# Kernel tuning notes

Measured on AMD Instinct MI355X. Metric: run time of the kernel, lower is better.

The kernel has to match this reference:

```python
import jax, jax.numpy as jnp
import numpy as np

B, N, D, OUT, ED = 8, 256, 128, 128, 1

def setup_inputs() -> dict:
    key = jax.random.key(0)
    ks = jax.random.split(key, 10)
    in2 = 2 * D + ED  # 257
    s = lambda f: 1.0 / np.sqrt(f)
    return {
        "h": jax.random.normal(ks[0], (B, N, D), dtype=jnp.float32),
        "adj": jax.random.randint(ks[1], (B, N, N), 0, 2, dtype=jnp.int32),
        "dist_matrix": jax.random.uniform(ks[2], (B, N, N), dtype=jnp.float32),
        "Wm1": jax.random.uniform(ks[3], (in2, OUT), minval=-s(in2), maxval=s(in2)),
        "bm1": jnp.zeros((OUT,), jnp.float32),
        "Wm2": jax.random.uniform(ks[4], (OUT, OUT), minval=-s(OUT), maxval=s(OUT)),
        "bm2": jnp.zeros((OUT,), jnp.float32),
        "Wa": jax.random.uniform(ks[5], (in2, 1), minval=-s(in2), maxval=s(in2)),
        "ba": jnp.zeros((1,), jnp.float32),
        "Wu": jax.random.uniform(ks[6], (D + OUT, OUT), minval=-s(D + OUT), maxval=s(D + OUT)),
        "bu": jnp.zeros((OUT,), jnp.float32),
    }

def reference(h, adj, dist_matrix, Wm1, bm1, Wm2, bm2, Wa, ba, Wu, bu):
    # h: (B,N,D); adj,dist: (B,N,N)
    Bb, Nn, Dd = h.shape
    h_i = jnp.broadcast_to(h[:, :, None, :], (Bb, Nn, Nn, Dd))
    h_j = jnp.broadcast_to(h[:, None, :, :], (Bb, Nn, Nn, Dd))
    d_ij = dist_matrix[..., None]
    msg_input = jnp.concatenate([h_i, h_j, d_ij], axis=-1)  # (B,N,N,2D+1)
    # message MLP: Linear -> ReLU -> Linear
    msg = jax.nn.relu(msg_input @ Wm1 + bm1) @ Wm2 + bm2    # (B,N,N,OUT)
    # attention MLP: Linear -> LeakyReLU(0.2)
    attn = jax.nn.leaky_relu(msg_input @ Wa + ba, 0.2)      # (B,N,N,1)
    mask = adj[..., None].astype(msg.dtype)                  # (B,N,N,1)
    attn = jnp.where(mask == 0, jnp.asarray(-1e9, attn.dtype), attn)
    attn = jax.nn.softmax(attn, axis=2)                      # softmax over j
    agg = jnp.sum(attn * msg * mask, axis=2)                 # (B,N,OUT)
    h_new = jax.nn.relu(jnp.concatenate([h, agg], axis=-1) @ Wu + bu)
    return h_new
```

## Files before the change

### kernel.cpp

```cpp
#include <hip/hip_runtime.h>

#define NN 256
#define DD 128
#define OC 128

__device__ __forceinline__ float bcastf(float x, int lane) {
    return __int_as_float(__builtin_amdgcn_readlane(__float_as_int(x), lane));
}

__global__ __launch_bounds__(256) void k1_pre(
    const float* __restrict__ h, const float* __restrict__ Wm1,
    const float* __restrict__ Wa, const float* __restrict__ bm1,
    const float* __restrict__ Wu, const float* __restrict__ ba,
    float* __restrict__ pre, float* __restrict__ aiv, float* __restrict__ ajv)
{
    const int tid  = threadIdx.x;
    const int l    = tid & 63;
    const int w    = tid >> 6;
    const int row0 = blockIdx.x * 4;

    const float2* h2 = (const float2*)h;
    float2 hr[4];
    #pragma unroll
    for (int r = 0; r < 4; ++r) hr[r] = h2[(row0 + r) * 64 + l];

    if (w == 3) {
        const float2* Wa2 = (const float2*)Wa;
        const float2 wt = Wa2[l], wb = Wa2[64 + l];
        float vi[4], vj[4];
        #pragma unroll
        for (int r = 0; r < 4; ++r) {
            vi[r] = hr[r].x * wt.x + hr[r].y * wt.y;
            vj[r] = hr[r].x * wb.x + hr[r].y * wb.y;
        }
        #pragma unroll
        for (int o = 1; o < 64; o <<= 1) {
            #pragma unroll
            for (int r = 0; r < 4; ++r) {
                vi[r] += __shfl_xor(vi[r], o, 64);
                vj[r] += __shfl_xor(vj[r], o, 64);
            }
        }
        if (l == 0) {
            const float b0 = ba[0];
            #pragma unroll
            for (int r = 0; r < 4; ++r) {
                aiv[row0 + r] = vi[r] + b0;
                ajv[row0 + r] = vj[r];
            }
        }
        return;
    }

    const float2* W2 = (w == 0) ? (const float2*)Wm1
                     : (w == 1) ? (const float2*)Wm1 + DD * 64
                                : (const float2*)Wu;

    float2 acc[4];
    #pragma unroll
    for (int r = 0; r < 4; ++r) acc[r] = make_float2(0.f, 0.f);

    #pragma unroll 4
    for (int m = 0; m < 64; ++m) {
        const float2 w0 = W2[(2 * m) * 64 + l];
        const float2 w1 = W2[(2 * m + 1) * 64 + l];
        #pragma unroll
        for (int r = 0; r < 4; ++r) {
            const float hx = bcastf(hr[r].x, m);
            const float hy = bcastf(hr[r].y, m);
            acc[r].x = fmaf(hx, w0.x, fmaf(hy, w1.x, acc[r].x));
            acc[r].y = fmaf(hx, w0.y, fmaf(hy, w1.y, acc[r].y));
        }
    }
    if (w == 0) {
        const float2 bb = ((const float2*)bm1)[l];
        #pragma unroll
        for (int r = 0; r < 4; ++r) { acc[r].x += bb.x; acc[r].y += bb.y; }
    }
    float2* pre2 = (float2*)pre;
    #pragma unroll
    for (int r = 0; r < 4; ++r)
        pre2[(row0 + r) * 192 + w * 64 + l] = acc[r];
}

__global__ __launch_bounds__(256) void k2_main(
    const int* __restrict__ adj, const float* __restrict__ dist,
    const float* __restrict__ Wm1, const float* __restrict__ Wa,
    const float* __restrict__ pre,
    const float* __restrict__ aiv, const float* __restrict__ ajv,
    const float* __restrict__ Wm2, const float* __restrict__ bm2,
    const float* __restrict__ Wu,  const float* __restrict__ bu,
    float* __restrict__ out)
{
    const int tid  = threadIdx.x;
    const int l    = tid & 63;
    const int w    = tid >> 6;
    const int row0 = blockIdx.x * 4;
    const int row  = row0 + w;
    const int b    = row >> 8;

    __shared__ float t_sh[4][128];
    __shared__ float agg_sh[4][128];
    __shared__ float sf_sh[4];

    const int4   mk4 = ((const int4*)  (adj  + row * NN))[l];
    const float4 dv4 = ((const float4*)(dist + row * NN))[l];
    const float4 aj4 = ((const float4*)(ajv  + b   * NN))[l];
    const float  ai  = aiv[row];
    const float  dc  = Wa[2 * DD];

    float lg[4];
    lg[0] = ai + aj4.x + dv4.x * dc;
    lg[1] = ai + aj4.y + dv4.y * dc;
    lg[2] = ai + aj4.z + dv4.z * dc;
    lg[3] = ai + aj4.w + dv4.w * dc;
    #pragma unroll
    for (int c = 0; c < 4; ++c) lg[c] = (lg[c] >= 0.f) ? lg[c] : 0.2f * lg[c];
    const int mk[4] = {mk4.x, mk4.y, mk4.z, mk4.w};

    float m = -1e9f;
    #pragma unroll
    for (int c = 0; c < 4; ++c) if (mk[c]) m = fmaxf(m, lg[c]);
    #pragma unroll
    for (int o = 1; o < 64; o <<= 1) m = fmaxf(m, __shfl_xor(m, o, 64));

    float e[4], s = 0.f;
    #pragma unroll
    for (int c = 0; c < 4; ++c) { e[c] = mk[c] ? __expf(lg[c] - m) : 0.f; s += e[c]; }
    #pragma unroll
    for (int o = 1; o < 64; o <<= 1) s += __shfl_xor(s, o, 64);
    const float inv = (s > 0.f) ? (1.0f / s) : 0.f;
    float wj0 = e[0] * inv, wj1 = e[1] * inv, wj2 = e[2] * inv, wj3 = e[3] * inv;

    const float2* pre2 = (const float2*)pre;
    const float2  pa   = pre2[row * 192 + l];
    const float2  wd1  = ((const float2*)Wm1)[2 * DD * 64 + l];
    const float2* pBb  = pre2 + (size_t)b * NN * 192 + 64;

    float2 acc = make_float2(0.f, 0.f);
    for (int p = 0; p < 64; ++p) {
        const float sw0 = bcastf(wj0, p), sd0 = bcastf(dv4.x, p);
        const float sw1 = bcastf(wj1, p), sd1 = bcastf(dv4.y, p);
        const float sw2 = bcastf(wj2, p), sd2 = bcastf(dv4.z, p);
        const float sw3 = bcastf(wj3, p), sd3 = bcastf(dv4.w, p);
        const int jb = 4 * p;
        if (sw0 != 0.f) {
            const float2 pb = pBb[jb * 192 + l];
            const float vx = fmaf(sd0, wd1.x, pa.x + pb.x);
            const float vy = fmaf(sd0, wd1.y, pa.y + pb.y);
            acc.x = fmaf(sw0, fmaxf(vx, 0.f), acc.x);
            acc.y = fmaf(sw0, fmaxf(vy, 0.f), acc.y);
        }
        if (sw1 != 0.f) {
            const float2 pb = pBb[(jb + 1) * 192 + l];
            const float vx = fmaf(sd1, wd1.x, pa.x + pb.x);
            const float vy = fmaf(sd1, wd1.y, pa.y + pb.y);
            acc.x = fmaf(sw1, fmaxf(vx, 0.f), acc.x);
            acc.y = fmaf(sw1, fmaxf(vy, 0.f), acc.y);
        }
        if (sw2 != 0.f) {
            const float2 pb = pBb[(jb + 2) * 192 + l];
            const float vx = fmaf(sd2, wd1.x, pa.x + pb.x);
            const float vy = fmaf(sd2, wd1.y, pa.y + pb.y);
            acc.x = fmaf(sw2, fmaxf(vx, 0.f), acc.x);
            acc.y = fmaf(sw2, fmaxf(vy, 0.f), acc.y);
        }
        if (sw3 != 0.f) {
            const float2 pb = pBb[(jb + 3) * 192 + l];
            const float vx = fmaf(sd3, wd1.x, pa.x + pb.x);
            const float vy = fmaf(sd3, wd1.y, pa.y + pb.y);
            acc.x = fmaf(sw3, fmaxf(vx, 0.f), acc.x);
            acc.y = fmaf(sw3, fmaxf(vy, 0.f), acc.y);
        }
    }
    t_sh[w][2 * l]     = acc.x;
    t_sh[w][2 * l + 1] = acc.y;
    if (l == 0) sf_sh[w] = (s > 0.f) ? 1.f : 0.f;
    __syncthreads();

    const int c   = 32 * w + (l & 31);
    const int rsl = l >> 5;
    float a[2];
    #pragma unroll
    for (int pass = 0; pass < 2; ++pass) {
        const int r = 2 * pass + rsl;
        float av = 0.f;
        #pragma unroll 8
        for (int k = 0; k < 128; ++k)
            av = fmaf(t_sh[r][k], Wm2[k * OC + c], av);
        a[pass] = fmaf(bm2[c], sf_sh[r], av);
    }
    #pragma unroll
    for (int pass = 0; pass < 2; ++pass)
        agg_sh[2 * pass + rsl][c] = a[pass];
    __syncthreads();

    const float buc = bu[c];
    #pragma unroll
    for (int pass = 0; pass < 2; ++pass) {
        const int r = 2 * pass + rsl;
        float ov = 0.f;
        #pragma unroll 8
        for (int k = 0; k < 128; ++k)
            ov = fmaf(agg_sh[r][k], Wu[(DD + k) * OC + c], ov);
        const float hu = pre[(row0 + r) * 384 + 256 + c];
        out[(row0 + r) * OC + c] = fmaxf(ov + hu + buc, 0.f);
    }
}

extern "C" void kernel_launch(void* const* d_in, const int* in_sizes, int n_in,
                              void* d_out, int out_size, void* d_ws, size_t ws_size,
                              hipStream_t stream) {
    const float* h    = (const float*)d_in[0];
    const int*   adj  = (const int*)  d_in[1];
    const float* dist = (const float*)d_in[2];
    const float* Wm1  = (const float*)d_in[3];
    const float* bm1  = (const float*)d_in[4];
    const float* Wm2  = (const float*)d_in[5];
    const float* bm2  = (const float*)d_in[6];
    const float* Wa   = (const float*)d_in[7];
    const float* ba   = (const float*)d_in[8];
    const float* Wu   = (const float*)d_in[9];
    const float* bu   = (const float*)d_in[10];
    float* out = (float*)d_out;

    float* pre = (float*)d_ws;
    float* aiv = pre + 2048 * 384;
    float* ajv = aiv + 2048;

    k1_pre <<<512, 256, 0, stream>>>(h, Wm1, Wa, bm1, Wu, ba, pre, aiv, ajv);
    k2_main<<<512, 256, 0, stream>>>(adj, dist, Wm1, Wa, pre, aiv, ajv,
                                     Wm2, bm2, Wu, bu, out);
}
```

Before: 132.2 us.

## Split each row's neighbor loop across two waves and double the grid

```diff
diff --git a/kernel.cpp b/kernel.cpp
--- a/kernel.cpp
+++ b/kernel.cpp
@@ -17,26 +17,26 @@
     const int tid  = threadIdx.x;
     const int l    = tid & 63;
     const int w    = tid >> 6;
-    const int row0 = blockIdx.x * 4;
+    const int row0 = blockIdx.x * 2;
 
     const float2* h2 = (const float2*)h;
-    float2 hr[4];
-    #pragma unroll
-    for (int r = 0; r < 4; ++r) hr[r] = h2[(row0 + r) * 64 + l];
+    float2 hr[2];
+    hr[0] = h2[row0 * 64 + l];
+    hr[1] = h2[(row0 + 1) * 64 + l];
 
     if (w == 3) {
         const float2* Wa2 = (const float2*)Wa;
         const float2 wt = Wa2[l], wb = Wa2[64 + l];
-        float vi[4], vj[4];
-        #pragma unroll
-        for (int r = 0; r < 4; ++r) {
+        float vi[2], vj[2];
+        #pragma unroll
+        for (int r = 0; r < 2; ++r) {
             vi[r] = hr[r].x * wt.x + hr[r].y * wt.y;
             vj[r] = hr[r].x * wb.x + hr[r].y * wb.y;
         }
         #pragma unroll
         for (int o = 1; o < 64; o <<= 1) {
             #pragma unroll
-            for (int r = 0; r < 4; ++r) {
+            for (int r = 0; r < 2; ++r) {
                 vi[r] += __shfl_xor(vi[r], o, 64);
                 vj[r] += __shfl_xor(vj[r], o, 64);
             }
@@ -44,7 +44,7 @@
         if (l == 0) {
             const float b0 = ba[0];
             #pragma unroll
-            for (int r = 0; r < 4; ++r) {
+            for (int r = 0; r < 2; ++r) {
                 aiv[row0 + r] = vi[r] + b0;
                 ajv[row0 + r] = vj[r];
             }
@@ -56,16 +56,13 @@
                      : (w == 1) ? (const float2*)Wm1 + DD * 64
                                 : (const float2*)Wu;
 
-    float2 acc[4];
-    #pragma unroll
-    for (int r = 0; r < 4; ++r) acc[r] = make_float2(0.f, 0.f);
-
-    #pragma unroll 4
+    float2 acc[2] = {{0.f, 0.f}, {0.f, 0.f}};
+    #pragma unroll 8
     for (int m = 0; m < 64; ++m) {
         const float2 w0 = W2[(2 * m) * 64 + l];
         const float2 w1 = W2[(2 * m + 1) * 64 + l];
         #pragma unroll
-        for (int r = 0; r < 4; ++r) {
+        for (int r = 0; r < 2; ++r) {
             const float hx = bcastf(hr[r].x, m);
             const float hy = bcastf(hr[r].y, m);
             acc[r].x = fmaf(hx, w0.x, fmaf(hy, w1.x, acc[r].x));
@@ -75,11 +72,11 @@
     if (w == 0) {
         const float2 bb = ((const float2*)bm1)[l];
         #pragma unroll
-        for (int r = 0; r < 4; ++r) { acc[r].x += bb.x; acc[r].y += bb.y; }
+        for (int r = 0; r < 2; ++r) { acc[r].x += bb.x; acc[r].y += bb.y; }
     }
     float2* pre2 = (float2*)pre;
     #pragma unroll
-    for (int r = 0; r < 4; ++r)
+    for (int r = 0; r < 2; ++r)
         pre2[(row0 + r) * 192 + w * 64 + l] = acc[r];
 }
 
@@ -94,118 +91,95 @@
 {
     const int tid  = threadIdx.x;
     const int l    = tid & 63;
-    const int w    = tid >> 6;
-    const int row0 = blockIdx.x * 4;
-    const int row  = row0 + w;
+    const int wid  = tid >> 6;
+    const int r    = wid >> 1;
+    const int hf   = wid & 1;
+    const int row0 = blockIdx.x * 2;
+    const int row  = row0 + r;
     const int b    = row >> 8;
 
-    __shared__ float t_sh[4][128];
-    __shared__ float agg_sh[4][128];
-    __shared__ float sf_sh[4];
-
-    const int4   mk4 = ((const int4*)  (adj  + row * NN))[l];
-    const float4 dv4 = ((const float4*)(dist + row * NN))[l];
-    const float4 aj4 = ((const float4*)(ajv  + b   * NN))[l];
+    __shared__ float mx_sh[4], sm_sh[4], sf_sh[2];
+    __shared__ float tp_sh[4][128];
+    __shared__ float t_sh[2][128];
+    __shared__ float agg_sh[2][128];
+
+    const float2 dv2 = ((const float2*)(dist + row * NN))[hf * 64 + l];
+    const int2   mk2 = ((const int2*)  (adj  + row * NN))[hf * 64 + l];
+    const float2 aj2 = ((const float2*)(ajv  + b   * NN))[hf * 64 + l];
     const float  ai  = aiv[row];
     const float  dc  = Wa[2 * DD];
 
-    float lg[4];
-    lg[0] = ai + aj4.x + dv4.x * dc;
-    lg[1] = ai + aj4.y + dv4.y * dc;
-    lg[2] = ai + aj4.z + dv4.z * dc;
-    lg[3] = ai + aj4.w + dv4.w * dc;
-    #pragma unroll
-    for (int c = 0; c < 4; ++c) lg[c] = (lg[c] >= 0.f) ? lg[c] : 0.2f * lg[c];
-    const int mk[4] = {mk4.x, mk4.y, mk4.z, mk4.w};
-
-    float m = -1e9f;
-    #pragma unroll
-    for (int c = 0; c < 4; ++c) if (mk[c]) m = fmaxf(m, lg[c]);
+    float l0 = ai + aj2.x + dv2.x * dc;
+    float l1 = ai + aj2.y + dv2.y * dc;
+    l0 = (l0 >= 0.f) ? l0 : 0.2f * l0;
+    l1 = (l1 >= 0.f) ? l1 : 0.2f * l1;
+
+    float m = fmaxf(mk2.x ? l0 : -1e9f, mk2.y ? l1 : -1e9f);
     #pragma unroll
     for (int o = 1; o < 64; o <<= 1) m = fmaxf(m, __shfl_xor(m, o, 64));
-
-    float e[4], s = 0.f;
-    #pragma unroll
-    for (int c = 0; c < 4; ++c) { e[c] = mk[c] ? __expf(lg[c] - m) : 0.f; s += e[c]; }
+    if (l == 0) mx_sh[wid] = m;
+    __syncthreads();
+    const float mx = fmaxf(mx_sh[r * 2], mx_sh[r * 2 + 1]);
+
+    const float e0 = mk2.x ? __expf(l0 - mx) : 0.f;
+    const float e1 = mk2.y ? __expf(l1 - mx) : 0.f;
+    float s = e0 + e1;
     #pragma unroll
     for (int o = 1; o < 64; o <<= 1) s += __shfl_xor(s, o, 64);
-    const float inv = (s > 0.f) ? (1.0f / s) : 0.f;
-    float wj0 = e[0] * inv, wj1 = e[1] * inv, wj2 = e[2] * inv, wj3 = e[3] * inv;
+    if (l == 0) sm_sh[wid] = s;
+    __syncthreads();
+    const float esum = sm_sh[r * 2] + sm_sh[r * 2 + 1];
+    const float inv  = (esum > 0.f) ? (1.0f / esum) : 0.f;
+    const float w0 = e0 * inv, w1 = e1 * inv;
 
     const float2* pre2 = (const float2*)pre;
     const float2  pa   = pre2[row * 192 + l];
     const float2  wd1  = ((const float2*)Wm1)[2 * DD * 64 + l];
-    const float2* pBb  = pre2 + (size_t)b * NN * 192 + 64;
+    const float2* pBb  = pre2 + (size_t)b * NN * 192 + 64 + (size_t)hf * 128 * 192;
 
     float2 acc = make_float2(0.f, 0.f);
+    #pragma unroll 8
     for (int p = 0; p < 64; ++p) {
-        const float sw0 = bcastf(wj0, p), sd0 = bcastf(dv4.x, p);
-        const float sw1 = bcastf(wj1, p), sd1 = bcastf(dv4.y, p);
-        const float sw2 = bcastf(wj2, p), sd2 = bcastf(dv4.z, p);
-        const float sw3 = bcastf(wj3, p), sd3 = bcastf(dv4.w, p);
-        const int jb = 4 * p;
-        if (sw0 != 0.f) {
-            const float2 pb = pBb[jb * 192 + l];
-            const float vx = fmaf(sd0, wd1.x, pa.x + pb.x);
-            const float vy = fmaf(sd0, wd1.y, pa.y + pb.y);
-            acc.x = fmaf(sw0, fmaxf(vx, 0.f), acc.x);
-            acc.y = fmaf(sw0, fmaxf(vy, 0.f), acc.y);
-        }
-        if (sw1 != 0.f) {
-            const float2 pb = pBb[(jb + 1) * 192 + l];
-            const float vx = fmaf(sd1, wd1.x, pa.x + pb.x);
-            const float vy = fmaf(sd1, wd1.y, pa.y + pb.y);
-            acc.x = fmaf(sw1, fmaxf(vx, 0.f), acc.x);
-            acc.y = fmaf(sw1, fmaxf(vy, 0.f), acc.y);
-        }
-        if (sw2 != 0.f) {
-            const float2 pb = pBb[(jb + 2) * 192 + l];
-            const float vx = fmaf(sd2, wd1.x, pa.x + pb.x);
-            const float vy = fmaf(sd2, wd1.y, pa.y + pb.y);
-            acc.x = fmaf(sw2, fmaxf(vx, 0.f), acc.x);
-            acc.y = fmaf(sw2, fmaxf(vy, 0.f), acc.y);
-        }
-        if (sw3 != 0.f) {
-            const float2 pb = pBb[(jb + 3) * 192 + l];
-            const float vx = fmaf(sd3, wd1.x, pa.x + pb.x);
-            const float vy = fmaf(sd3, wd1.y, pa.y + pb.y);
-            acc.x = fmaf(sw3, fmaxf(vx, 0.f), acc.x);
-            acc.y = fmaf(sw3, fmaxf(vy, 0.f), acc.y);
-        }
-    }
-    t_sh[w][2 * l]     = acc.x;
-    t_sh[w][2 * l + 1] = acc.y;
-    if (l == 0) sf_sh[w] = (s > 0.f) ? 1.f : 0.f;
-    __syncthreads();
-
-    const int c   = 32 * w + (l & 31);
-    const int rsl = l >> 5;
-    float a[2];
-    #pragma unroll
-    for (int pass = 0; pass < 2; ++pass) {
-        const int r = 2 * pass + rsl;
-        float av = 0.f;
-        #pragma unroll 8
-        for (int k = 0; k < 128; ++k)
-            av = fmaf(t_sh[r][k], Wm2[k * OC + c], av);
-        a[pass] = fmaf(bm2[c], sf_sh[r], av);
-    }
-    #pragma unroll
-    for (int pass = 0; pass < 2; ++pass)
-        agg_sh[2 * pass + rsl][c] = a[pass];
-    __syncthreads();
-
-    const float buc = bu[c];
-    #pragma unroll
-    for (int pass = 0; pass < 2; ++pass) {
-        const int r = 2 * pass + rsl;
-        float ov = 0.f;
-        #pragma unroll 8
-        for (int k = 0; k < 128; ++k)
-            ov = fmaf(agg_sh[r][k], Wu[(DD + k) * OC + c], ov);
-        const float hu = pre[(row0 + r) * 384 + 256 + c];
-        out[(row0 + r) * OC + c] = fmaxf(ov + hu + buc, 0.f);
-    }
+        const float w0p = bcastf(w0, p);
+        const float w1p = bcastf(w1, p);
+        const float d0p = bcastf(dv2.x, p);
+        const float d1p = bcastf(dv2.y, p);
+        const float2 pb0 = pBb[(2 * p) * 192 + l];
+        const float2 pb1 = pBb[(2 * p + 1) * 192 + l];
+        float vx = fmaf(d0p, wd1.x, pa.x + pb0.x);
+        float vy = fmaf(d0p, wd1.y, pa.y + pb0.y);
+        acc.x = fmaf(w0p, fmaxf(vx, 0.f), acc.x);
+        acc.y = fmaf(w0p, fmaxf(vy, 0.f), acc.y);
+        vx = fmaf(d1p, wd1.x, pa.x + pb1.x);
+        vy = fmaf(d1p, wd1.y, pa.y + pb1.y);
+        acc.x = fmaf(w1p, fmaxf(vx, 0.f), acc.x);
+        acc.y = fmaf(w1p, fmaxf(vy, 0.f), acc.y);
+    }
+    tp_sh[wid][2 * l]     = acc.x;
+    tp_sh[wid][2 * l + 1] = acc.y;
+    if (l == 0 && hf == 0) sf_sh[r] = (esum > 0.f) ? 1.f : 0.f;
+    __syncthreads();
+
+    {
+        const int rr = tid >> 7, cc = tid & 127;
+        t_sh[rr][cc] = tp_sh[rr * 2][cc] + tp_sh[rr * 2 + 1][cc];
+    }
+    __syncthreads();
+
+    const int r2 = tid >> 7, c = tid & 127;
+    float av = 0.f;
+    #pragma unroll 8
+    for (int k = 0; k < 128; ++k)
+        av = fmaf(t_sh[r2][k], Wm2[k * OC + c], av);
+    agg_sh[r2][c] = fmaf(bm2[c], sf_sh[r2], av);
+    __syncthreads();
+
+    float ov = 0.f;
+    #pragma unroll 8
+    for (int k = 0; k < 128; ++k)
+        ov = fmaf(agg_sh[r2][k], Wu[(DD + k) * OC + c], ov);
+    const float hu = pre[(row0 + r2) * 384 + 256 + c];
+    out[(row0 + r2) * OC + c] = fmaxf(ov + hu + bu[c], 0.f);
 }
 
 extern "C" void kernel_launch(void* const* d_in, const int* in_sizes, int n_in,
@@ -228,7 +202,7 @@
     float* aiv = pre + 2048 * 384;
     float* ajv = aiv + 2048;
 
-    k1_pre <<<512, 256, 0, stream>>>(h, Wm1, Wa, bm1, Wu, ba, pre, aiv, ajv);
-    k2_main<<<512, 256, 0, stream>>>(adj, dist, Wm1, Wa, pre, aiv, ajv,
-                                     Wm2, bm2, Wu, bu, out);
-}
+    k1_pre <<<1024, 256, 0, stream>>>(h, Wm1, Wa, bm1, Wu, ba, pre, aiv, ajv);
+    k2_main<<<1024, 256, 0, stream>>>(adj, dist, Wm1, Wa, pre, aiv, ajv,
+                                      Wm2, bm2, Wu, bu, out);
+}
```

Result: faster. 116.4 us (-11.9%).
